# Kernel optimization log

Hardware: AMD Instinct MI355X
Metric: run time of the kernel (lower is better)

Reference implementation:

```python
import jax, jax.numpy as jnp
import numpy as np

N_DAYS, N_HOURS, N_LINKS, N_FEAT = 4, 24, 2000, 4
N_ODS, PATHS_PER_OD = 5000, 4
N_PATHS = N_ODS * PATHS_PER_OD
LINK_DENSITY = 0.005  # ~10 links per path in the path-link incidence D


def setup_inputs() -> dict:
    key = jax.random.key(0)
    ks = jax.random.split(key, 6)
    # X: (days, hours, links, 1 + n_features); channel 0 is free-flow travel time (stripped)
    X = jax.random.normal(ks[0], (N_DAYS, N_HOURS, N_LINKS, N_FEAT + 1), jnp.float32)
    theta = jax.random.normal(ks[1], (N_FEAT,), jnp.float32) * 0.5
    theta_links = jax.random.normal(ks[2], (N_LINKS,), jnp.float32) * 0.1
    # model stores sqrt(q); demand q = sqrt_q**2
    sqrt_q = jax.random.uniform(ks[3], (N_ODS,), jnp.float32, minval=0.5, maxval=2.0)
    # path size factors in (0, 1]
    psf = jax.random.uniform(ks[4], (N_PATHS,), jnp.float32, minval=0.5, maxval=1.0)
    psc_factor = jnp.zeros((1,), jnp.float32)  # init 0, as in the module
    # D: binary path-link incidence (n_links, n_paths)
    D = (jax.random.uniform(ks[5], (N_LINKS, N_PATHS)) < LINK_DENSITY).astype(jnp.float32)
    # each OD has exactly PATHS_PER_OD consecutive paths (sorted segment ids)
    path_od = jnp.repeat(jnp.arange(N_ODS, dtype=jnp.int32), PATHS_PER_OD)
    return dict(X=X, theta=theta, theta_links=theta_links, sqrt_q=sqrt_q,
                psf=psf, psc_factor=psc_factor, D=D, path_od=path_od)


def reference(X, theta, theta_links, sqrt_q, psf, psc_factor, D, path_od):
    # predict_flow: strip tt_ff channel, then ODLUE.call, then relu
    feat = X[..., 1:]                                   # (d, h, L, F)
    # link utilities: einsum('ijkl,l->ijk') + theta_links
    V = jnp.einsum('dhlf,f->dhl', feat, theta) + theta_links
    # path utilities with path-size correction: einsum('ijk,kl->ijl', V, D) + psc*log(psf)
    Vf = jnp.einsum('dhl,lp->dhp', V, D) + psc_factor[0] * jnp.log(psf)  # (d, h, P)
    d, h, P = Vf.shape
    n_ods = sqrt_q.shape[0]
    # per-OD softmax over paths (sparse normalization: segment max is stop-gradient'd)
    Vt = Vf.reshape(d * h, P).T                         # (P, B)
    vmax = jax.lax.stop_gradient(
        jax.ops.segment_max(Vt, path_od, num_segments=n_ods))  # (n_ods, B)
    ev = jnp.exp(Vt - vmax[path_od])                    # (P, B)
    denom = jax.ops.segment_sum(ev, path_od, num_segments=n_ods)  # (n_ods, B)
    pf = (ev / denom[path_od]).T.reshape(d, h, P)       # path probabilities
    # path flows: demand of each path's OD times its probability
    q = sqrt_q ** 2
    f = pf * q[path_od]                                 # (d, h, P)
    # link flows: einsum('ijk,lk->ijl', f, D)
    link_flow = jnp.einsum('dhp,lp->dhl', f, D)         # (d, h, L)
    return jax.nn.relu(link_flow)
```

## Files before the change

### kernel.cpp

```cpp
#include <hip/hip_runtime.h>
#include <cstdint>
#include <cstddef>

#define NT   96
#define NL   2000
#define NP   20000
#define NOD  5000
#define NF   4
#define CAP_P 64
#define CAP_L 256

#define OFF_CNTP 0
#define OFF_CNTL 80000
#define OFF_VT   88064
#define OFF_IDXP 856064
#define OFF_IDXL 3416064
#define OFF_FT   4440064

__global__ void k_V(const float* __restrict__ X, const float* __restrict__ theta,
                    const float* __restrict__ theta_links, float* __restrict__ V_T,
                    uint32_t* __restrict__ cntP) {
    int i = blockIdx.x * blockDim.x + threadIdx.x;
    if (i < NP) cntP[i] = 0u;
    if (i >= NT * NL) return;
    int t = i / NL;
    int l = i - t * NL;
    const float* x = X + (size_t)i * (NF + 1) + 1;
    float v = x[0] * theta[0] + x[1] * theta[1] + x[2] * theta[2] + x[3] * theta[3]
            + theta_links[l];
    V_T[(size_t)l * NT + t] = v;
}

__global__ __launch_bounds__(256) void k_extract(const float* __restrict__ D,
                          uint32_t* __restrict__ cntP, uint32_t* __restrict__ cntL,
                          uint16_t* __restrict__ idxP, uint16_t* __restrict__ idxL) {
    const int l = blockIdx.x;
    __shared__ uint32_t lcnt;
    if (threadIdx.x == 0) lcnt = 0;
    __syncthreads();
    const float4* row = (const float4*)(D + (size_t)l * NP);
#pragma unroll 4
    for (int i = 0; i < 20; ++i) {
        int g = threadIdx.x + i * 256;
        if (g >= NP / 4) break;
        float4 v = row[g];
        float vals[4] = {v.x, v.y, v.z, v.w};
#pragma unroll
        for (int j = 0; j < 4; ++j) {
            if (vals[j] != 0.f) {
                int p = g * 4 + j;
                uint32_t slot = atomicAdd(&lcnt, 1u);
                if (slot < CAP_L) idxL[(size_t)l * CAP_L + slot] = (uint16_t)p;
                uint32_t sp = atomicAdd(&cntP[p], 1u);
                if (sp < CAP_P) idxP[(size_t)p * CAP_P + sp] = (uint16_t)l;
            }
        }
    }
    __syncthreads();
    if (threadIdx.x == 0) cntL[l] = (lcnt > CAP_L) ? CAP_L : lcnt;
}

__global__ void k_path(const float* __restrict__ V_T, const uint32_t* __restrict__ cntP,
                       const uint16_t* __restrict__ idxP, const float* __restrict__ psf,
                       const float* __restrict__ sqrt_q, const float* __restrict__ psc,
                       float* __restrict__ f_T) {
    int od = blockIdx.x;
    int t  = threadIdx.x;
    if (t >= NT) return;
    float pscf = psc[0];
    float vf[4];
#pragma unroll
    for (int j = 0; j < 4; ++j) {
        int p = od * 4 + j;
        float acc = pscf * logf(psf[p]);
        uint32_t c = cntP[p];
        if (c > CAP_P) c = CAP_P;
        const uint16_t* lst = idxP + (size_t)p * CAP_P;
        for (uint32_t k = 0; k < c; ++k) {
            int l = lst[k];
            acc += V_T[(size_t)l * NT + t];
        }
        vf[j] = acc;
    }
    float m = fmaxf(fmaxf(vf[0], vf[1]), fmaxf(vf[2], vf[3]));
    float e0 = __expf(vf[0] - m), e1 = __expf(vf[1] - m);
    float e2 = __expf(vf[2] - m), e3 = __expf(vf[3] - m);
    float sq = sqrt_q[od];
    float s  = (sq * sq) / (e0 + e1 + e2 + e3);
    f_T[(size_t)(od * 4 + 0) * NT + t] = e0 * s;
    f_T[(size_t)(od * 4 + 1) * NT + t] = e1 * s;
    f_T[(size_t)(od * 4 + 2) * NT + t] = e2 * s;
    f_T[(size_t)(od * 4 + 3) * NT + t] = e3 * s;
}

__global__ void k_gather(const float* __restrict__ f_T, const uint32_t* __restrict__ cntL,
                         const uint16_t* __restrict__ idxL, float* __restrict__ out) {
    int l = blockIdx.x;
    int t = threadIdx.x;
    if (t >= NT) return;
    uint32_t c = cntL[l];
    const uint16_t* lst = idxL + (size_t)l * CAP_L;
    float s = 0.f;
    for (uint32_t k = 0; k < c; ++k) {
        int p = lst[k];
        s += f_T[(size_t)p * NT + t];
    }
    out[(size_t)t * NL + l] = fmaxf(s, 0.f);
}

extern "C" void kernel_launch(void* const* d_in, const int* in_sizes, int n_in,
                              void* d_out, int out_size, void* d_ws, size_t ws_size,
                              hipStream_t stream) {
    const float* X           = (const float*)d_in[0];
    const float* theta       = (const float*)d_in[1];
    const float* theta_links = (const float*)d_in[2];
    const float* sqrt_q      = (const float*)d_in[3];
    const float* psf         = (const float*)d_in[4];
    const float* psc         = (const float*)d_in[5];
    const float* D           = (const float*)d_in[6];
    float* out = (float*)d_out;

    char* ws = (char*)d_ws;
    uint32_t* cntP = (uint32_t*)(ws + OFF_CNTP);
    uint32_t* cntL = (uint32_t*)(ws + OFF_CNTL);
    float*    V_T  = (float*)   (ws + OFF_VT);
    uint16_t* idxP = (uint16_t*)(ws + OFF_IDXP);
    uint16_t* idxL = (uint16_t*)(ws + OFF_IDXL);
    float*    f_T  = (float*)   (ws + OFF_FT);

    k_V      <<<(NT * NL + 255) / 256, 256, 0, stream>>>(X, theta, theta_links, V_T, cntP);
    k_extract<<<NL, 256, 0, stream>>>(D, cntP, cntL, idxP, idxL);
    k_path   <<<NOD, 128, 0, stream>>>(V_T, cntP, idxP, psf, sqrt_q, psc, f_T);
    k_gather <<<NL, 128, 0, stream>>>(f_T, cntL, idxL, out);
}
```

Measured before the change: 131.6 us.

## Split CSR extraction and inversion; pack two ODs/links per block

The path-side atomic inversion moves out of the dense D scan into a separate kernel that reads the compact per-link index lists. The D scan also skips float4 groups that are all zero. k_path and k_gather now handle two rows per 192-thread block, so no threads sit idle in the 128-thread blocks. This adds one more kernel launch and changes the order of entries in the per-path lists, which may alter the floating-point summation order slightly.

```diff
diff --git a/kernel.cpp b/kernel.cpp
--- a/kernel.cpp
+++ b/kernel.cpp
@@ -32,27 +32,21 @@
 }
 
 __global__ __launch_bounds__(256) void k_extract(const float* __restrict__ D,
-                          uint32_t* __restrict__ cntP, uint32_t* __restrict__ cntL,
-                          uint16_t* __restrict__ idxP, uint16_t* __restrict__ idxL) {
+                          uint32_t* __restrict__ cntL, uint16_t* __restrict__ idxL) {
     const int l = blockIdx.x;
     __shared__ uint32_t lcnt;
     if (threadIdx.x == 0) lcnt = 0;
     __syncthreads();
     const float4* row = (const float4*)(D + (size_t)l * NP);
-#pragma unroll 4
-    for (int i = 0; i < 20; ++i) {
-        int g = threadIdx.x + i * 256;
-        if (g >= NP / 4) break;
+    for (int g = threadIdx.x; g < NP / 4; g += 256) {
         float4 v = row[g];
+        if (v.x == 0.f && v.y == 0.f && v.z == 0.f && v.w == 0.f) continue;
         float vals[4] = {v.x, v.y, v.z, v.w};
 #pragma unroll
         for (int j = 0; j < 4; ++j) {
             if (vals[j] != 0.f) {
-                int p = g * 4 + j;
                 uint32_t slot = atomicAdd(&lcnt, 1u);
-                if (slot < CAP_L) idxL[(size_t)l * CAP_L + slot] = (uint16_t)p;
-                uint32_t sp = atomicAdd(&cntP[p], 1u);
-                if (sp < CAP_P) idxP[(size_t)p * CAP_P + sp] = (uint16_t)l;
+                if (slot < CAP_L) idxL[(size_t)l * CAP_L + slot] = (uint16_t)(g * 4 + j);
             }
         }
     }
@@ -60,13 +54,26 @@
     if (threadIdx.x == 0) cntL[l] = (lcnt > CAP_L) ? CAP_L : lcnt;
 }
 
-__global__ void k_path(const float* __restrict__ V_T, const uint32_t* __restrict__ cntP,
+__global__ __launch_bounds__(256) void k_invert(const uint32_t* __restrict__ cntL,
+                          const uint16_t* __restrict__ idxL,
+                          uint32_t* __restrict__ cntP, uint16_t* __restrict__ idxP) {
+    int l = blockIdx.x;
+    uint32_t c = cntL[l];
+    uint32_t s = threadIdx.x;
+    if (s >= c) return;
+    int p = idxL[(size_t)l * CAP_L + s];
+    uint32_t sp = atomicAdd(&cntP[p], 1u);
+    if (sp < CAP_P) idxP[(size_t)p * CAP_P + sp] = (uint16_t)l;
+}
+
+__global__ __launch_bounds__(192) void k_path(const float* __restrict__ V_T,
+                       const uint32_t* __restrict__ cntP,
                        const uint16_t* __restrict__ idxP, const float* __restrict__ psf,
                        const float* __restrict__ sqrt_q, const float* __restrict__ psc,
                        float* __restrict__ f_T) {
-    int od = blockIdx.x;
-    int t  = threadIdx.x;
-    if (t >= NT) return;
+    int half = threadIdx.x / 96;
+    int t    = threadIdx.x - half * 96;
+    int od   = blockIdx.x * 2 + half;
     float pscf = psc[0];
     float vf[4];
 #pragma unroll
@@ -93,11 +100,12 @@
     f_T[(size_t)(od * 4 + 3) * NT + t] = e3 * s;
 }
 
-__global__ void k_gather(const float* __restrict__ f_T, const uint32_t* __restrict__ cntL,
+__global__ __launch_bounds__(192) void k_gather(const float* __restrict__ f_T,
+                         const uint32_t* __restrict__ cntL,
                          const uint16_t* __restrict__ idxL, float* __restrict__ out) {
-    int l = blockIdx.x;
-    int t = threadIdx.x;
-    if (t >= NT) return;
+    int half = threadIdx.x / 96;
+    int t    = threadIdx.x - half * 96;
+    int l    = blockIdx.x * 2 + half;
     uint32_t c = cntL[l];
     const uint16_t* lst = idxL + (size_t)l * CAP_L;
     float s = 0.f;
@@ -129,7 +137,8 @@
     float*    f_T  = (float*)   (ws + OFF_FT);
 
     k_V      <<<(NT * NL + 255) / 256, 256, 0, stream>>>(X, theta, theta_links, V_T, cntP);
-    k_extract<<<NL, 256, 0, stream>>>(D, cntP, cntL, idxP, idxL);
-    k_path   <<<NOD, 128, 0, stream>>>(V_T, cntP, idxP, psf, sqrt_q, psc, f_T);
-    k_gather <<<NL, 128, 0, stream>>>(f_T, cntL, idxL, out);
+    k_extract<<<NL, 256, 0, stream>>>(D, cntL, idxL);
+    k_invert <<<NL, 256, 0, stream>>>(cntL, idxL, cntP, idxP);
+    k_path   <<<NOD / 2, 192, 0, stream>>>(V_T, cntP, idxP, psf, sqrt_q, psc, f_T);
+    k_gather <<<NL / 2, 192, 0, stream>>>(f_T, cntL, idxL, out);
 }
```

Result: faster. 126.8 us (-3.6%).
